# Optimization experiments

Hardware: AMD Instinct MI355X
Metric: run time of the kernel (lower is better)

## Reference

```python
import jax, jax.numpy as jnp
import numpy as np

E = 8            # moe_num_experts
FFN = 8192       # ffn_hidden_size
D = 2048         # d_model
B, T = 1, 4096


def setup_inputs() -> dict:
    key = jax.random.key(0)
    k1, k2, k3, k4 = jax.random.split(key, 4)
    x = jax.random.normal(k1, (B, T, D), dtype=jnp.float32)
    # params stored flat as (E*FFN, D), as in the flax module
    w1 = jax.random.normal(k2, (E * FFN, D), dtype=jnp.float32) * 0.02
    v1 = jax.random.normal(k3, (E * FFN, D), dtype=jnp.float32) * 0.02
    w2 = jax.random.normal(k4, (E * FFN, D), dtype=jnp.float32) * 0.02
    return {"x": x, "w1": w1, "v1": v1, "w2": w2, "expert_idx": 3}


def reference(x, w1, v1, w2, expert_idx):
    # select this expert's weight slabs: (FFN, D) each
    expert_shape = (E, FFN, D)
    ew1 = w1.reshape(expert_shape)[expert_idx]
    ev1 = v1.reshape(expert_shape)[expert_idx]
    ew2 = w2.reshape(expert_shape)[expert_idx]
    # gate and up projections: [B,T,D] x [D,FFN] -> [B,T,FFN]
    x1 = jnp.einsum('btd,fd->btf', x, ew1)
    x2 = jnp.einsum('btd,fd->btf', x, ev1)
    h = jax.nn.silu(x1) * x2
    # down projection (note: matmul with ew2, i.e. contraction over FFN)
    out = jnp.einsum('btf,fd->btd', h, ew2)
    return out
```

## Files before the change

kernel.cpp:

```cpp
#include <hip/hip_runtime.h>

#define E_NUM 8
#define FFN_DIM 8192
#define D_DIM 2048
#define T_DIM 4096

using bf16x8 = __attribute__((ext_vector_type(8))) short;
using f32x4  = __attribute__((ext_vector_type(4))) float;
using u16x8  = __attribute__((ext_vector_type(8))) unsigned short;

__device__ __forceinline__ unsigned short f2bf(float f) {
  union { float f; unsigned int u; } v; v.f = f;
  unsigned int u = v.u;
  unsigned int r = (u + 0x7FFFu + ((u >> 16) & 1u)) >> 16;
  return (unsigned short)r;
}

__device__ __forceinline__ void gload16(const unsigned short* g, const unsigned short* l) {
  __builtin_amdgcn_global_load_lds(
      (const __attribute__((address_space(1))) void*)g,
      (__attribute__((address_space(3))) void*)l, 16, 0, 0);
}

__global__ void convert_kernel(const float* __restrict__ src_base,
                               const int* __restrict__ eidx, long slab,
                               unsigned short* __restrict__ dst, long n) {
  const float* src = src_base + (long)(*eidx) * slab;
  long stride = (long)gridDim.x * blockDim.x;
  for (long i = (long)blockIdx.x * blockDim.x + threadIdx.x; i * 8 < n; i += stride) {
    long e = i * 8;
    const float4* p = (const float4*)(src + e);
    float4 f0 = p[0], f1 = p[1];
    u16x8 o;
    o[0] = f2bf(f0.x); o[1] = f2bf(f0.y); o[2] = f2bf(f0.z); o[3] = f2bf(f0.w);
    o[4] = f2bf(f1.x); o[5] = f2bf(f1.y); o[6] = f2bf(f1.z); o[7] = f2bf(f1.w);
    *(u16x8*)(dst + e) = o;
  }
}

__global__ void transpose_kernel(const float* __restrict__ w2,
                                 const int* __restrict__ eidx,
                                 unsigned short* __restrict__ dst) {
  __shared__ unsigned short tile[32][33];
  const float* src = w2 + (long)(*eidx) * (long)FFN_DIM * D_DIM;
  int d0 = blockIdx.x << 5;
  int f0 = blockIdx.y << 5;
  int tx = threadIdx.x & 31, ty = threadIdx.x >> 5;
#pragma unroll
  for (int i = 0; i < 4; ++i) {
    int f = ty + i * 8;
    tile[f][tx] = f2bf(src[(long)(f0 + f) * D_DIM + d0 + tx]);
  }
  __syncthreads();
#pragma unroll
  for (int i = 0; i < 4; ++i) {
    int d = ty + i * 8;
    dst[(long)(d0 + d) * FFN_DIM + f0 + tx] = tile[tx][d];
  }
}

#define VMCNT6 asm volatile("s_waitcnt vmcnt(6)" ::: "memory")
#define VMCNT4 asm volatile("s_waitcnt vmcnt(4)" ::: "memory")
#define VMCNT0 asm volatile("s_waitcnt vmcnt(0)" ::: "memory")
#define BAR __builtin_amdgcn_s_barrier()
#define PRIO1 __builtin_amdgcn_s_setprio(1)
#define PRIO0 __builtin_amdgcn_s_setprio(0)

__global__ __launch_bounds__(512, 2) void gemm1_silu(
    const unsigned short* __restrict__ Xb,
    const unsigned short* __restrict__ W1b,
    const unsigned short* __restrict__ V1b,
    unsigned short* __restrict__ Hb) {
  __shared__ __align__(16) unsigned short sA[2 * 2 * 8192];
  __shared__ __align__(16) unsigned short sB1[2 * 8192];
  __shared__ __align__(16) unsigned short sB2[2 * 8192];

  const int tid = threadIdx.x;
  const int wv = tid >> 6, l = tid & 63;
  const int wm = wv >> 2, wn = wv & 3;
  const int kq = l >> 4, lr = l & 15;
  const int m0 = blockIdx.y << 8;
  const int n0 = blockIdx.x << 7;

  const int rsub = tid >> 3;
  const int sslot8 = ((tid & 7) ^ ((tid >> 3) & 7)) << 3;
  const unsigned short* gA  = Xb  + (long)(m0 + rsub) * D_DIM + sslot8;
  const unsigned short* gB1 = W1b + (long)(n0 + rsub) * D_DIM + sslot8;
  const unsigned short* gB2 = V1b + (long)(n0 + rsub) * D_DIM + sslot8;

#define STG(gbase, rowoff, tc_, lbase) do { \
    gload16((gbase) + (long)(rowoff) * D_DIM + (tc_), (lbase) + wv * 512); \
    gload16((gbase) + (long)((rowoff) + 64) * D_DIM + (tc_), (lbase) + 4096 + wv * 512); \
  } while (0)

  int aoff[4], boff[2];
#pragma unroll
  for (int j = 0; j < 4; ++j) {
    int row = wm * 64 + j * 16 + lr;
    aoff[j] = row * 64 + ((kq ^ (row & 7)) << 3);
  }
#pragma unroll
  for (int g = 0; g < 2; ++g) {
    int row = wn * 32 + g * 16 + lr;
    boff[g] = row * 64 + ((kq ^ (row & 7)) << 3);
  }

  f32x4 acc1[8][2], acc2[8][2];
  f32x4 z = {0.f, 0.f, 0.f, 0.f};
#pragma unroll
  for (int f = 0; f < 8; ++f)
#pragma unroll
    for (int g = 0; g < 2; ++g) { acc1[f][g] = z; acc2[f][g] = z; }

  STG(gA, 0, 0, sA);
  STG(gA, 128, 0, sA + 8192);
  STG(gB1, 0, 0, sB1);
  STG(gB2, 0, 0, sB2);
  STG(gA, 0, 64, sA + 16384);
  STG(gA, 128, 64, sA + 24576);
  STG(gB1, 0, 64, sB1 + 8192);
  VMCNT6;
  BAR;

  const int NT = D_DIM / 64;
  for (int t = 0; t < NT; ++t) {
    const int db = t & 1, sx = db ^ 1;
    const unsigned short* A0p = sA + (db * 2 + 0) * 8192;
    const unsigned short* A1p = sA + (db * 2 + 1) * 8192;
    const unsigned short* B1p = sB1 + db * 8192;
    const unsigned short* B2p = sB2 + db * 8192;
    const int p1ok = (t + 1 < NT), p2ok = (t + 2 < NT);
    const int tc1 = (t + 1) << 6, tc2 = (t + 2) << 6;
    bf16x8 aA[4][2], aB[4][2], b1[2][2], b2[2][2];

#pragma unroll
    for (int j = 0; j < 4; ++j) {
      aA[j][0] = *(const bf16x8*)(A0p + aoff[j]);
      aA[j][1] = *(const bf16x8*)(A0p + (aoff[j] ^ 32));
    }
#pragma unroll
    for (int g = 0; g < 2; ++g) {
      b1[g][0] = *(const bf16x8*)(B1p + boff[g]);
      b1[g][1] = *(const bf16x8*)(B1p + (boff[g] ^ 32));
    }
    if (p1ok) STG(gB2, 0, tc1, sB2 + sx * 8192);
    BAR;
    PRIO1;
#pragma unroll
    for (int j = 0; j < 4; ++j)
#pragma unroll
      for (int g = 0; g < 2; ++g) {
        acc1[j][g] = __builtin_amdgcn_mfma_f32_16x16x32_bf16(aA[j][0], b1[g][0], acc1[j][g], 0, 0, 0);
        acc1[j][g] = __builtin_amdgcn_mfma_f32_16x16x32_bf16(aA[j][1], b1[g][1], acc1[j][g], 0, 0, 0);
      }
    PRIO0;
    BAR;

#pragma unroll
    for (int j = 0; j < 4; ++j) {
      aB[j][0] = *(const bf16x8*)(A1p + aoff[j]);
      aB[j][1] = *(const bf16x8*)(A1p + (aoff[j] ^ 32));
    }
    if (p2ok) STG(gA, 0, tc2, sA + (db * 2 + 0) * 8192);
    BAR;
    PRIO1;
#pragma unroll
    for (int j = 0; j < 4; ++j)
#pragma unroll
      for (int g = 0; g < 2; ++g) {
        acc1[4 + j][g] = __builtin_amdgcn_mfma_f32_16x16x32_bf16(aB[j][0], b1[g][0], acc1[4 + j][g], 0, 0, 0);
        acc1[4 + j][g] = __builtin_amdgcn_mfma_f32_16x16x32_bf16(aB[j][1], b1[g][1], acc1[4 + j][g], 0, 0, 0);
      }
    PRIO0;
    BAR;

#pragma unroll
    for (int g = 0; g < 2; ++g) {
      b2[g][0] = *(const bf16x8*)(B2p + boff[g]);
      b2[g][1] = *(const bf16x8*)(B2p + (boff[g] ^ 32));
    }
    if (p2ok) STG(gA, 128, tc2, sA + (db * 2 + 1) * 8192);
    BAR;
    PRIO1;
#pragma unroll
    for (int j = 0; j < 4; ++j)
#pragma unroll
      for (int g = 0; g < 2; ++g) {
        acc2[j][g] = __builtin_amdgcn_mfma_f32_16x16x32_bf16(aA[j][0], b2[g][0], acc2[j][g], 0, 0, 0);
        acc2[j][g] = __builtin_amdgcn_mfma_f32_16x16x32_bf16(aA[j][1], b2[g][1], acc2[j][g], 0, 0, 0);
      }
    PRIO0;
    BAR;

    if (p2ok) STG(gB1, 0, tc2, sB1 + db * 8192);
    BAR;
    PRIO1;
#pragma unroll
    for (int j = 0; j < 4; ++j)
#pragma unroll
      for (int g = 0; g < 2; ++g) {
        acc2[4 + j][g] = __builtin_amdgcn_mfma_f32_16x16x32_bf16(aB[j][0], b2[g][0], acc2[4 + j][g], 0, 0, 0);
        acc2[4 + j][g] = __builtin_amdgcn_mfma_f32_16x16x32_bf16(aB[j][1], b2[g][1], acc2[4 + j][g], 0, 0, 0);
      }
    PRIO0;
    if (p2ok) { VMCNT6; } else if (p1ok) { VMCNT0; }
    BAR;
  }

#pragma unroll
  for (int f = 0; f < 8; ++f)
#pragma unroll
    for (int g = 0; g < 2; ++g)
#pragma unroll
      for (int r = 0; r < 4; ++r) {
        int row = m0 + (f >> 2) * 128 + wm * 64 + (f & 3) * 16 + kq * 4 + r;
        int col = n0 + wn * 32 + g * 16 + lr;
        float x1 = acc1[f][g][r], x2 = acc2[f][g][r];
        float hv = x1 / (1.f + __expf(-x1)) * x2;
        Hb[(long)row * FFN_DIM + col] = f2bf(hv);
      }
#undef STG
}

__global__ __launch_bounds__(512, 2) void gemm2(
    const unsigned short* __restrict__ Hb,
    const unsigned short* __restrict__ W2T,
    float* __restrict__ out) {
  __shared__ __align__(16) unsigned short sA[2 * 2 * 8192];
  __shared__ __align__(16) unsigned short sB[2 * 8192];

  const int tid = threadIdx.x;
  const int wv = tid >> 6, l = tid & 63;
  const int wm = wv >> 1, wn = wv & 1;
  const int kq = l >> 4, lr = l & 15;
  const int m0 = blockIdx.y << 8;
  const int n0 = blockIdx.x << 7;
  const int hA = wm >> 1;

  const int rsub = tid >> 3;
  const int sslot8 = ((tid & 7) ^ ((tid >> 3) & 7)) << 3;
  const unsigned short* gA = Hb  + (long)(m0 + rsub) * FFN_DIM + sslot8;
  const unsigned short* gB = W2T + (long)(n0 + rsub) * FFN_DIM + sslot8;

#define STG2(gbase, rowoff, tc_, lbase) do { \
    gload16((gbase) + (long)(rowoff) * FFN_DIM + (tc_), (lbase) + wv * 512); \
    gload16((gbase) + (long)((rowoff) + 64) * FFN_DIM + (tc_), (lbase) + 4096 + wv * 512); \
  } while (0)

  int aoff[4], boff[4];
#pragma unroll
  for (int f = 0; f < 4; ++f) {
    int row = (wm & 1) * 64 + f * 16 + lr;
    aoff[f] = row * 64 + ((kq ^ (row & 7)) << 3);
  }
#pragma unroll
  for (int g = 0; g < 4; ++g) {
    int row = wn * 64 + g * 16 + lr;
    boff[g] = row * 64 + ((kq ^ (row & 7)) << 3);
  }

  f32x4 acc[4][4];
  f32x4 z = {0.f, 0.f, 0.f, 0.f};
#pragma unroll
  for (int f = 0; f < 4; ++f)
#pragma unroll
    for (int g = 0; g < 4; ++g) acc[f][g] = z;

  STG2(gA, 0, 0, sA);
  STG2(gA, 128, 0, sA + 8192);
  STG2(gB, 0, 0, sB);
  STG2(gA, 0, 64, sA + 16384);
  STG2(gA, 128, 64, sA + 24576);
  VMCNT4;
  BAR;

  const int NT = FFN_DIM / 64;
  for (int t = 0; t < NT; ++t) {
    const int db = t & 1, sx = db ^ 1;
    const unsigned short* Ap = sA + (db * 2 + hA) * 8192;
    const unsigned short* Bp = sB + db * 8192;
    const int p1ok = (t + 1 < NT), p2ok = (t + 2 < NT);
    const int tc1 = (t + 1) << 6, tc2 = (t + 2) << 6;
    bf16x8 aA[2][2], aB[2][2], bA[2][2], bB[2][2];

#pragma unroll
    for (int f = 0; f < 2; ++f) {
      aA[f][0] = *(const bf16x8*)(Ap + aoff[f]);
      aA[f][1] = *(const bf16x8*)(Ap + (aoff[f] ^ 32));
    }
#pragma unroll
    for (int g = 0; g < 2; ++g) {
      bA[g][0] = *(const bf16x8*)(Bp + boff[g]);
      bA[g][1] = *(const bf16x8*)(Bp + (boff[g] ^ 32));
    }
    if (p1ok) STG2(gB, 0, tc1, sB + sx * 8192);
    BAR;
    PRIO1;
#pragma unroll
    for (int f = 0; f < 2; ++f)
#pragma unroll
      for (int g = 0; g < 2; ++g) {
        acc[f][g] = __builtin_amdgcn_mfma_f32_16x16x32_bf16(aA[f][0], bA[g][0], acc[f][g], 0, 0, 0);
        acc[f][g] = __builtin_amdgcn_mfma_f32_16x16x32_bf16(aA[f][1], bA[g][1], acc[f][g], 0, 0, 0);
      }
    PRIO0;
    BAR;

#pragma unroll
    for (int f = 0; f < 2; ++f) {
      aB[f][0] = *(const bf16x8*)(Ap + aoff[2 + f]);
      aB[f][1] = *(const bf16x8*)(Ap + (aoff[2 + f] ^ 32));
    }
    BAR;
    PRIO1;
#pragma unroll
    for (int f = 0; f < 2; ++f)
#pragma unroll
      for (int g = 0; g < 2; ++g) {
        acc[2 + f][g] = __builtin_amdgcn_mfma_f32_16x16x32_bf16(aB[f][0], bA[g][0], acc[2 + f][g], 0, 0, 0);
        acc[2 + f][g] = __builtin_amdgcn_mfma_f32_16x16x32_bf16(aB[f][1], bA[g][1], acc[2 + f][g], 0, 0, 0);
      }
    PRIO0;
    BAR;

#pragma unroll
    for (int g = 0; g < 2; ++g) {
      bB[g][0] = *(const bf16x8*)(Bp + boff[2 + g]);
      bB[g][1] = *(const bf16x8*)(Bp + (boff[2 + g] ^ 32));
    }
    if (p2ok) STG2(gA, 0, tc2, sA + (db * 2 + 0) * 8192);
    BAR;
    PRIO1;
#pragma unroll
    for (int f = 0; f < 2; ++f)
#pragma unroll
      for (int g = 0; g < 2; ++g) {
        acc[f][2 + g] = __builtin_amdgcn_mfma_f32_16x16x32_bf16(aA[f][0], bB[g][0], acc[f][2 + g], 0, 0, 0);
        acc[f][2 + g] = __builtin_amdgcn_mfma_f32_16x16x32_bf16(aA[f][1], bB[g][1], acc[f][2 + g], 0, 0, 0);
      }
    PRIO0;
    BAR;

    if (p2ok) STG2(gA, 128, tc2, sA + (db * 2 + 1) * 8192);
    BAR;
    PRIO1;
#pragma unroll
    for (int f = 0; f < 2; ++f)
#pragma unroll
      for (int g = 0; g < 2; ++g) {
        acc[2 + f][2 + g] = __builtin_amdgcn_mfma_f32_16x16x32_bf16(aB[f][0], bB[g][0], acc[2 + f][2 + g], 0, 0, 0);
        acc[2 + f][2 + g] = __builtin_amdgcn_mfma_f32_16x16x32_bf16(aB[f][1], bB[g][1], acc[2 + f][2 + g], 0, 0, 0);
      }
    PRIO0;
    if (p2ok) { VMCNT4; } else if (p1ok) { VMCNT0; }
    BAR;
  }

#pragma unroll
  for (int f = 0; f < 4; ++f)
#pragma unroll
    for (int g = 0; g < 4; ++g)
#pragma unroll
      for (int r = 0; r < 4; ++r) {
        int row = m0 + wm * 64 + f * 16 + kq * 4 + r;
        int col = n0 + wn * 64 + g * 16 + lr;
        out[(long)row * D_DIM + col] = acc[f][g][r];
      }
#undef STG2
}

extern "C" void kernel_launch(void* const* d_in, const int* in_sizes, int n_in,
                              void* d_out, int out_size, void* d_ws, size_t ws_size,
                              hipStream_t stream) {
  const float* x  = (const float*)d_in[0];
  const float* w1 = (const float*)d_in[1];
  const float* v1 = (const float*)d_in[2];
  const float* w2 = (const float*)d_in[3];
  const int* eidx = (const int*)d_in[4];

  char* ws = (char*)d_ws;
  unsigned short* Xb  = (unsigned short*)(ws);
  unsigned short* W1b = (unsigned short*)(ws + (16l << 20));
  unsigned short* V1b = (unsigned short*)(ws + (48l << 20));
  unsigned short* W2T = (unsigned short*)(ws + (80l << 20));
  unsigned short* Hb  = (unsigned short*)(ws + (112l << 20));
  float* out = (float*)d_out;

  long slab = (long)FFN_DIM * D_DIM;
  convert_kernel<<<2048, 256, 0, stream>>>(x,  eidx, 0,    Xb,  (long)T_DIM * D_DIM);
  convert_kernel<<<2048, 256, 0, stream>>>(w1, eidx, slab, W1b, slab);
  convert_kernel<<<2048, 256, 0, stream>>>(v1, eidx, slab, V1b, slab);
  transpose_kernel<<<dim3(D_DIM / 32, FFN_DIM / 32), 256, 0, stream>>>(w2, eidx, W2T);
  gemm1_silu<<<dim3(FFN_DIM / 128, T_DIM / 256), 512, 0, stream>>>(Xb, W1b, V1b, Hb);
  gemm2<<<dim3(D_DIM / 128, T_DIM / 256), 512, 0, stream>>>(Hb, W2T, out);
}
```

Baseline: 491.6 us.

## Swizzle block order for XCD locality and prefetch B tiles two steps ahead

Both GEMMs now use a 1D grid whose block index is remapped so that each group of eight consecutive blocks (one per XCD round-robin slot) covers contiguous M tiles sharing the same N columns, aiming at better L2 reuse of weight tiles. The B-operand loads are moved from a one-step lookahead into the same two-step-ahead prefetch schedule as A, with vmcnt waits raised to match. Launch order of the conversion kernels is also shuffled. The deeper prefetch keeps more loads in flight but changes the barrier/vmcnt accounting, which must stay consistent with the LDS double-buffer reuse.

```diff
diff --git a/kernel.cpp b/kernel.cpp
--- a/kernel.cpp
+++ b/kernel.cpp
@@ -59,8 +59,8 @@
   }
 }
 
+#define VMCNT8 asm volatile("s_waitcnt vmcnt(8)" ::: "memory")
 #define VMCNT6 asm volatile("s_waitcnt vmcnt(6)" ::: "memory")
-#define VMCNT4 asm volatile("s_waitcnt vmcnt(4)" ::: "memory")
 #define VMCNT0 asm volatile("s_waitcnt vmcnt(0)" ::: "memory")
 #define BAR __builtin_amdgcn_s_barrier()
 #define PRIO1 __builtin_amdgcn_s_setprio(1)
@@ -79,8 +79,9 @@
   const int wv = tid >> 6, l = tid & 63;
   const int wm = wv >> 2, wn = wv & 3;
   const int kq = l >> 4, lr = l & 15;
-  const int m0 = blockIdx.y << 8;
-  const int n0 = blockIdx.x << 7;
+  const int bsw = (blockIdx.x & 7) * 128 + (blockIdx.x >> 3);
+  const int m0 = (bsw & 15) << 8;
+  const int n0 = (bsw >> 4) << 7;
 
   const int rsub = tid >> 3;
   const int sslot8 = ((tid & 7) ^ ((tid >> 3) & 7)) << 3;
@@ -119,18 +120,19 @@
   STG(gA, 0, 64, sA + 16384);
   STG(gA, 128, 64, sA + 24576);
   STG(gB1, 0, 64, sB1 + 8192);
-  VMCNT6;
+  STG(gB2, 0, 64, sB2 + 8192);
+  VMCNT8;
   BAR;
 
   const int NT = D_DIM / 64;
   for (int t = 0; t < NT; ++t) {
-    const int db = t & 1, sx = db ^ 1;
+    const int db = t & 1;
     const unsigned short* A0p = sA + (db * 2 + 0) * 8192;
     const unsigned short* A1p = sA + (db * 2 + 1) * 8192;
     const unsigned short* B1p = sB1 + db * 8192;
     const unsigned short* B2p = sB2 + db * 8192;
     const int p1ok = (t + 1 < NT), p2ok = (t + 2 < NT);
-    const int tc1 = (t + 1) << 6, tc2 = (t + 2) << 6;
+    const int tc2 = (t + 2) << 6;
     bf16x8 aA[4][2], aB[4][2], b1[2][2], b2[2][2];
 
 #pragma unroll
@@ -143,7 +145,6 @@
       b1[g][0] = *(const bf16x8*)(B1p + boff[g]);
       b1[g][1] = *(const bf16x8*)(B1p + (boff[g] ^ 32));
     }
-    if (p1ok) STG(gB2, 0, tc1, sB2 + sx * 8192);
     BAR;
     PRIO1;
 #pragma unroll
@@ -161,7 +162,10 @@
       aB[j][0] = *(const bf16x8*)(A1p + aoff[j]);
       aB[j][1] = *(const bf16x8*)(A1p + (aoff[j] ^ 32));
     }
-    if (p2ok) STG(gA, 0, tc2, sA + (db * 2 + 0) * 8192);
+    if (p2ok) {
+      STG(gA, 0, tc2, sA + (db * 2 + 0) * 8192);
+      STG(gB1, 0, tc2, sB1 + db * 8192);
+    }
     BAR;
     PRIO1;
 #pragma unroll
@@ -192,7 +196,7 @@
     PRIO0;
     BAR;
 
-    if (p2ok) STG(gB1, 0, tc2, sB1 + db * 8192);
+    if (p2ok) STG(gB2, 0, tc2, sB2 + db * 8192);
     BAR;
     PRIO1;
 #pragma unroll
@@ -203,7 +207,7 @@
         acc2[4 + j][g] = __builtin_amdgcn_mfma_f32_16x16x32_bf16(aB[j][1], b2[g][1], acc2[4 + j][g], 0, 0, 0);
       }
     PRIO0;
-    if (p2ok) { VMCNT6; } else if (p1ok) { VMCNT0; }
+    if (p2ok) { VMCNT8; } else if (p1ok) { VMCNT0; }
     BAR;
   }
 
@@ -233,8 +237,9 @@
   const int wv = tid >> 6, l = tid & 63;
   const int wm = wv >> 1, wn = wv & 1;
   const int kq = l >> 4, lr = l & 15;
-  const int m0 = blockIdx.y << 8;
-  const int n0 = blockIdx.x << 7;
+  const int bsw = (blockIdx.x & 7) * 32 + (blockIdx.x >> 3);
+  const int m0 = (bsw & 15) << 8;
+  const int n0 = (bsw >> 4) << 7;
   const int hA = wm >> 1;
 
   const int rsub = tid >> 3;
@@ -271,16 +276,17 @@
   STG2(gB, 0, 0, sB);
   STG2(gA, 0, 64, sA + 16384);
   STG2(gA, 128, 64, sA + 24576);
-  VMCNT4;
+  STG2(gB, 0, 64, sB + 8192);
+  VMCNT6;
   BAR;
 
   const int NT = FFN_DIM / 64;
   for (int t = 0; t < NT; ++t) {
-    const int db = t & 1, sx = db ^ 1;
+    const int db = t & 1;
     const unsigned short* Ap = sA + (db * 2 + hA) * 8192;
     const unsigned short* Bp = sB + db * 8192;
     const int p1ok = (t + 1 < NT), p2ok = (t + 2 < NT);
-    const int tc1 = (t + 1) << 6, tc2 = (t + 2) << 6;
+    const int tc2 = (t + 2) << 6;
     bf16x8 aA[2][2], aB[2][2], bA[2][2], bB[2][2];
 
 #pragma unroll
@@ -293,7 +299,6 @@
       bA[g][0] = *(const bf16x8*)(Bp + boff[g]);
       bA[g][1] = *(const bf16x8*)(Bp + (boff[g] ^ 32));
     }
-    if (p1ok) STG2(gB, 0, tc1, sB + sx * 8192);
     BAR;
     PRIO1;
 #pragma unroll
@@ -328,7 +333,10 @@
       bB[g][0] = *(const bf16x8*)(Bp + boff[2 + g]);
       bB[g][1] = *(const bf16x8*)(Bp + (boff[2 + g] ^ 32));
     }
-    if (p2ok) STG2(gA, 0, tc2, sA + (db * 2 + 0) * 8192);
+    if (p2ok) {
+      STG2(gA, 0, tc2, sA + (db * 2 + 0) * 8192);
+      STG2(gA, 128, tc2, sA + (db * 2 + 1) * 8192);
+    }
     BAR;
     PRIO1;
 #pragma unroll
@@ -341,7 +349,7 @@
     PRIO0;
     BAR;
 
-    if (p2ok) STG2(gA, 128, tc2, sA + (db * 2 + 1) * 8192);
+    if (p2ok) STG2(gB, 0, tc2, sB + db * 8192);
     BAR;
     PRIO1;
 #pragma unroll
@@ -352,7 +360,7 @@
         acc[2 + f][2 + g] = __builtin_amdgcn_mfma_f32_16x16x32_bf16(aB[f][1], bB[g][1], acc[2 + f][2 + g], 0, 0, 0);
       }
     PRIO0;
-    if (p2ok) { VMCNT4; } else if (p1ok) { VMCNT0; }
+    if (p2ok) { VMCNT6; } else if (p1ok) { VMCNT0; }
     BAR;
   }
 
@@ -387,10 +395,10 @@
   float* out = (float*)d_out;
 
   long slab = (long)FFN_DIM * D_DIM;
-  convert_kernel<<<2048, 256, 0, stream>>>(x,  eidx, 0,    Xb,  (long)T_DIM * D_DIM);
+  transpose_kernel<<<dim3(D_DIM / 32, FFN_DIM / 32), 256, 0, stream>>>(w2, eidx, W2T);
   convert_kernel<<<2048, 256, 0, stream>>>(w1, eidx, slab, W1b, slab);
   convert_kernel<<<2048, 256, 0, stream>>>(v1, eidx, slab, V1b, slab);
-  transpose_kernel<<<dim3(D_DIM / 32, FFN_DIM / 32), 256, 0, stream>>>(w2, eidx, W2T);
-  gemm1_silu<<<dim3(FFN_DIM / 128, T_DIM / 256), 512, 0, stream>>>(Xb, W1b, V1b, Hb);
-  gemm2<<<dim3(D_DIM / 128, T_DIM / 256), 512, 0, stream>>>(Hb, W2T, out);
-}
+  convert_kernel<<<2048, 256, 0, stream>>>(x,  eidx, 0,    Xb,  (long)T_DIM * D_DIM);
+  gemm1_silu<<<1024, 512, 0, stream>>>(Xb, W1b, V1b, Hb);
+  gemm2<<<256, 512, 0, stream>>>(Hb, W2T, out);
+}
```

After: 490.6 us. About the same (-0.2%).
